# Kernel tuning notes

Measured on AMD Instinct MI355X. Metric: run time of the kernel, lower is better.

## Reference

```python
import jax, jax.numpy as jnp
import numpy as np

B, N, D = 32, 2048, 512

def setup_inputs() -> dict:
    key = jax.random.key(0)
    k1, k2, k3, k4 = jax.random.split(key, 4)
    return {
        "src": jax.random.normal(k1, (B, N, 3), dtype=jnp.float32),
        "tgt": jax.random.normal(k2, (B, N, 3), dtype=jnp.float32),
        "src_embed": jax.random.normal(k3, (B, N, D), dtype=jnp.float32),
        "tgt_embed": jax.random.normal(k4, (B, N, D), dtype=jnp.float32),
    }

def reference(src, tgt, src_embed, tgt_embed):
    # src, tgt: (B, N, 3); src_embed, tgt_embed: (B, N, D)
    d_k = jnp.asarray(src_embed.shape[-1], dtype=src_embed.dtype)
    # attention scores (B, N_src, N_tgt), softmax over tgt points
    scores = jnp.einsum('bnd,bmd->bnm', src_embed, tgt_embed) / jnp.sqrt(d_k)
    pointer = jax.nn.softmax(scores, axis=2)
    # matched = tgt^T @ pointer^T -> (B, 3, N_src)
    matched = jnp.einsum('bmc,bnm->bcn', tgt, pointer)
    src_t = jnp.transpose(src, (0, 2, 1))  # (B, 3, N)
    src_cent = jnp.mean(src_t, axis=2, keepdims=True)        # (B, 3, 1)
    matched_cent = jnp.mean(matched, axis=2, keepdims=True)  # (B, 3, 1)
    src_demean = src_t - src_cent
    matched_demean = matched - matched_cent
    # cross-covariance H: (B, 3, 3)
    H = jnp.einsum('bcn,bdn->bcd', src_demean, matched_demean)
    U, _, Vh = jnp.linalg.svd(H, full_matrices=False)  # square 3x3: reduced == full
    V = jnp.transpose(Vh, (0, 2, 1))
    R = jnp.matmul(V, jnp.transpose(U, (0, 2, 1)))
    det = jnp.linalg.det(R)
    identity = jnp.eye(3, dtype=R.dtype)
    reflect = jnp.diag(jnp.array([1.0, 1.0, -1.0], dtype=R.dtype))
    refl = jnp.where((det >= 0)[:, None, None], identity, reflect)
    R = jnp.matmul(refl, R)
    t = jnp.matmul(-R, src_cent) + matched_cent  # (B, 3, 1)
    t = jnp.transpose(t, (0, 2, 1))              # (B, 1, 3)
    return (R, t)
```

## Files before the change

kernel.cpp:

```cpp
#include <hip/hip_runtime.h>
#include <hip/hip_fp16.h>
#include <math.h>

#define B_ 32
#define N_ 2048
#define D_ 512
#define BN 128
#define NWAVE 8

typedef __attribute__((ext_vector_type(8))) _Float16 f16x8;
typedef __attribute__((ext_vector_type(8))) short s16x8;
typedef __attribute__((ext_vector_type(4))) float f32x4;
typedef __attribute__((ext_vector_type(4))) unsigned int u32x4;

__device__ inline unsigned packh2(float lo, float hi) {
    __half l = __float2half_rn(lo), h = __float2half_rn(hi);
    return (unsigned)__half_as_ushort(l) | ((unsigned)__half_as_ushort(h) << 16);
}
__device__ inline unsigned f2bf(float x) {
    unsigned u = __float_as_uint(x);
    return (u + 0x7FFFu + ((u >> 16) & 1u)) >> 16;
}
__device__ inline float bf2f(unsigned h) { return __uint_as_float(h << 16); }

__global__ __launch_bounds__(256) void prepass_kernel(
    const float* __restrict__ te, u32x4* __restrict__ kp)
{
    const int idx = blockIdx.x * 256 + threadIdx.x;
    const int b   = idx >> 17;
    const int r17 = idx & 131071;
    const int mt  = r17 >> 13;
    const int kt  = (r17 >> 9) & 15;
    const int o16 = r17 & 511;
    const int r   = o16 >> 2;
    const int s   = o16 & 3;
    const int lg  = s ^ ((r >> 1) & 3);
    const float* src = te + (((size_t)b * N_ + mt * 128 + r) * D_ + kt * 32 + lg * 8);
    const float4 f0 = *(const float4*)src;
    const float4 f1 = *(const float4*)(src + 4);
    u32x4 u;
    u[0] = packh2(f0.x, f0.y);
    u[1] = packh2(f0.z, f0.w);
    u[2] = packh2(f1.x, f1.y);
    u[3] = packh2(f1.z, f1.w);
    kp[idx] = u;
}

__global__ __launch_bounds__(512, 2) void attn_fast_kernel(
    const float* __restrict__ src, const float* __restrict__ tgt,
    const float* __restrict__ src_embed, const u32x4* __restrict__ kp,
    double* __restrict__ partials)
{
    __shared__ f16x8 Kbuf[2][512];
    __shared__ float4 TsB[2][BN];
    __shared__ double red[NWAVE][15];

    const int tid  = threadIdx.x;
    const int wv   = tid >> 6;
    const int lane = tid & 63;
    const int lr   = lane & 15;
    const int lg   = lane >> 4;

    const int xcd  = blockIdx.x & 7;
    const int slot = blockIdx.x >> 3;
    const int b    = xcd * 4 + (slot >> 3);
    const int msl  = slot & 7;
    const int n0   = msl * 256;
    const int pblk = b * 8 + msl;

    const int sx   = lg ^ ((lr >> 1) & 3);
    char* KbufB = (char*)&Kbuf[0][0];

    const float QSC = 0.044194173824159216f * 1.4426950408889634f;
    f16x8 Qr[2][16];
#pragma unroll
    for (int qf = 0; qf < 2; ++qf) {
        const int qrow = n0 + wv * 32 + qf * 16 + lr;
        const float* qp = src_embed + ((size_t)b * N_ + qrow) * D_ + lg * 8;
#pragma unroll
        for (int s = 0; s < 16; ++s) {
            const float4 f0 = *(const float4*)(qp + s * 32);
            const float4 f1 = *(const float4*)(qp + s * 32 + 4);
            u32x4 u;
            u[0] = packh2(f0.x * QSC, f0.y * QSC);
            u[1] = packh2(f0.z * QSC, f0.w * QSC);
            u[2] = packh2(f1.x * QSC, f1.y * QSC);
            u[3] = packh2(f1.z * QSC, f1.w * QSC);
            Qr[qf][s] = __builtin_bit_cast(f16x8, u);
        }
    }

#define TILEPTR(mt_, kt_) (kp + ((((size_t)b * 16 + (mt_)) * 16 + (kt_)) << 9) + tid)
#define STAGE(mt_, kt_, bufi_) \
    __builtin_amdgcn_global_load_lds( \
        (const __attribute__((address_space(1))) void*)TILEPTR(mt_, kt_), \
        (__attribute__((address_space(3))) void*)(&Kbuf[bufi_][wv * 64]), 16, 0, 0)

    float m_s[2] = {-1e30f, -1e30f}, l_s[2] = {0.f, 0.f};
    float axs[2] = {0.f, 0.f}, ays[2] = {0.f, 0.f}, azs[2] = {0.f, 0.f};

    STAGE(0, 0, 0);
    if (tid < BN) {
        const float* tp = tgt + ((size_t)b * N_ + tid) * 3;
        TsB[0][tid] = make_float4(tp[0], tp[1], tp[2], 0.f);
    }
    __syncthreads();

    for (int mc = 0; mc < 16; ++mc) {
        f32x4 acc[2][8];
#pragma unroll
        for (int qf = 0; qf < 2; ++qf)
#pragma unroll
            for (int nf = 0; nf < 8; ++nf) acc[qf][nf] = (f32x4){0.f, 0.f, 0.f, 0.f};

        float tv0 = 0.f, tv1 = 0.f, tv2 = 0.f;
#pragma unroll
        for (int kt = 0; kt < 16; ++kt) {
            const int cur = kt & 1;
            if (kt < 15)          { STAGE(mc,     kt + 1, cur ^ 1); }
            else if (mc < 15)     { STAGE(mc + 1, 0,      cur ^ 1); }
            if (kt == 0 && mc < 15 && tid < BN) {
                const float* tp = tgt + ((size_t)b * N_ + (mc + 1) * BN + tid) * 3;
                tv0 = tp[0]; tv1 = tp[1]; tv2 = tp[2];
            }
            const char* base = KbufB + cur * 8192 + lr * 64 + sx * 16;
#pragma unroll
            for (int nf = 0; nf < 8; ++nf) {
                const f16x8 a = *(const f16x8*)(base + nf * 1024);
                acc[0][nf] = __builtin_amdgcn_mfma_f32_16x16x32_f16(a, Qr[0][kt], acc[0][nf], 0, 0, 0);
                acc[1][nf] = __builtin_amdgcn_mfma_f32_16x16x32_f16(a, Qr[1][kt], acc[1][nf], 0, 0, 0);
            }
            if (kt == 0 && mc < 15 && tid < BN)
                TsB[(mc + 1) & 1][tid] = make_float4(tv0, tv1, tv2, 0.f);
            __syncthreads();
        }

        const float4* Ts = TsB[mc & 1];
        float mx0 = -1e30f, mx1 = -1e30f;
#pragma unroll
        for (int nf = 0; nf < 8; ++nf)
#pragma unroll
            for (int r4 = 0; r4 < 4; ++r4) {
                mx0 = fmaxf(mx0, acc[0][nf][r4]);
                mx1 = fmaxf(mx1, acc[1][nf][r4]);
            }
        mx0 = fmaxf(mx0, __shfl_xor(mx0, 16)); mx0 = fmaxf(mx0, __shfl_xor(mx0, 32));
        mx1 = fmaxf(mx1, __shfl_xor(mx1, 16)); mx1 = fmaxf(mx1, __shfl_xor(mx1, 32));
        const float mn0 = fmaxf(m_s[0], mx0), mn1 = fmaxf(m_s[1], mx1);
        const float c0 = exp2f(m_s[0] - mn0), c1 = exp2f(m_s[1] - mn1);
        l_s[0] *= c0; axs[0] *= c0; ays[0] *= c0; azs[0] *= c0; m_s[0] = mn0;
        l_s[1] *= c1; axs[1] *= c1; ays[1] *= c1; azs[1] *= c1; m_s[1] = mn1;
        float l0 = 0.f, x0 = 0.f, y0 = 0.f, z0 = 0.f;
        float l1 = 0.f, x1 = 0.f, y1 = 0.f, z1 = 0.f;
#pragma unroll
        for (int nf = 0; nf < 8; ++nf)
#pragma unroll
            for (int r4 = 0; r4 < 4; ++r4) {
                const float4 tv = Ts[nf * 16 + lg * 4 + r4];
                const float p0 = exp2f(acc[0][nf][r4] - mn0);
                const float p1 = exp2f(acc[1][nf][r4] - mn1);
                l0 += p0; x0 = fmaf(p0, tv.x, x0); y0 = fmaf(p0, tv.y, y0); z0 = fmaf(p0, tv.z, z0);
                l1 += p1; x1 = fmaf(p1, tv.x, x1); y1 = fmaf(p1, tv.y, y1); z1 = fmaf(p1, tv.z, z1);
            }
        l_s[0] += l0; axs[0] += x0; ays[0] += y0; azs[0] += z0;
        l_s[1] += l1; axs[1] += x1; ays[1] += y1; azs[1] += z1;
        __syncthreads();
    }

    double dl[15];
#pragma unroll
    for (int i = 0; i < 15; ++i) dl[i] = 0.0;
#pragma unroll
    for (int qf = 0; qf < 2; ++qf) {
        float lt = l_s[qf], x = axs[qf], y = ays[qf], z = azs[qf];
        lt += __shfl_xor(lt, 16); lt += __shfl_xor(lt, 32);
        x  += __shfl_xor(x, 16);  x  += __shfl_xor(x, 32);
        y  += __shfl_xor(y, 16);  y  += __shfl_xor(y, 32);
        z  += __shfl_xor(z, 16);  z  += __shfl_xor(z, 32);
        if (lg == 0) {
            const int qrow = n0 + wv * 32 + qf * 16 + lr;
            const float* sp = src + ((size_t)b * N_ + qrow) * 3;
            const double inv = 1.0 / (double)lt;
            const double m0d = (double)x * inv, m1d = (double)y * inv, m2d = (double)z * inv;
            const double s0 = sp[0], s1 = sp[1], s2 = sp[2];
            dl[0] += s0;  dl[1] += s1;  dl[2] += s2;
            dl[3] += m0d; dl[4] += m1d; dl[5] += m2d;
            dl[6]  += s0 * m0d; dl[7]  += s0 * m1d; dl[8]  += s0 * m2d;
            dl[9]  += s1 * m0d; dl[10] += s1 * m1d; dl[11] += s1 * m2d;
            dl[12] += s2 * m0d; dl[13] += s2 * m1d; dl[14] += s2 * m2d;
        }
    }
#pragma unroll
    for (int i = 0; i < 15; ++i) {
        double v = dl[i];
        for (int off = 1; off < 64; off <<= 1) v += __shfl_xor(v, off);
        dl[i] = v;
    }
    if (lane == 0) {
#pragma unroll
        for (int i = 0; i < 15; ++i) red[wv][i] = dl[i];
    }
    __syncthreads();
    if (tid < 15) {
        double sum = 0.0;
        for (int w = 0; w < NWAVE; ++w) sum += red[w][tid];
        partials[(size_t)pblk * 15 + tid] = sum;
    }
#undef STAGE
#undef TILEPTR
}

__global__ __launch_bounds__(256, 2) void attn_v2_kernel(
    const float* __restrict__ src, const float* __restrict__ tgt,
    const float* __restrict__ src_embed, const float* __restrict__ tgt_embed,
    double* __restrict__ partials)
{
    __shared__ short Khi_s[128 * 64];
    __shared__ short Klo_s[128 * 64];
    __shared__ float4 Ts4[128];
    __shared__ double red[64][15];

    char* KhiB = (char*)Khi_s;
    char* KloB = (char*)Klo_s;

    const int w    = blockIdx.x;
    const int xcd  = w & 7;
    const int idx  = w >> 3;
    const int b    = xcd * 4 + (idx >> 5);
    const int n0   = (idx & 31) * 64;
    const int blk  = b * 32 + (idx & 31);

    const int tid  = threadIdx.x;
    const int wv   = tid >> 6;
    const int lane = tid & 63;
    const int lr   = lane & 15;
    const int lg   = lane >> 4;
    const unsigned swl = (unsigned)((lr & 7) << 4);

    const float scale = 0.044194173824159216f;
    const float* kbase = tgt_embed + (size_t)b * N_ * D_;

    const int qrow = n0 + wv * 16 + lr;
    const float* qp = src_embed + ((size_t)b * N_ + qrow) * D_ + lg * 8;
    s16x8 qhi[16], qlo[16];
#pragma unroll
    for (int s = 0; s < 16; ++s) {
        const float4 f0 = *reinterpret_cast<const float4*>(qp + s * 32);
        const float4 f1 = *reinterpret_cast<const float4*>(qp + s * 32 + 4);
        const float x[8] = {f0.x, f0.y, f0.z, f0.w, f1.x, f1.y, f1.z, f1.w};
#pragma unroll
        for (int i = 0; i < 8; ++i) {
            const float v = x[i] * scale;
            const unsigned h = f2bf(v);
            qhi[s][i] = (short)h;
            qlo[s][i] = (short)f2bf(v - bf2f(h));
        }
    }

    float m_run = -1e30f, l_run = 0.f, a0 = 0.f, a1 = 0.f, a2 = 0.f;
    const int srow = tid >> 1;
    const int shalf = tid & 1;
    const unsigned swr = (unsigned)((srow & 7) << 4);

    for (int m0 = 0; m0 < N_; m0 += 128) {
        f32x4 acc[8];
#pragma unroll
        for (int nf = 0; nf < 8; ++nf) acc[nf] = (f32x4){0.f, 0.f, 0.f, 0.f};

#pragma unroll
        for (int kt = 0; kt < 8; ++kt) {
            __syncthreads();
            {
                const float* gp = kbase + (size_t)(m0 + srow) * D_ + kt * 64 + shalf * 32;
#pragma unroll
                for (int grp = 0; grp < 4; ++grp) {
                    const float4 fa = *reinterpret_cast<const float4*>(gp + grp * 8);
                    const float4 fb = *reinterpret_cast<const float4*>(gp + grp * 8 + 4);
                    const float x[8] = {fa.x, fa.y, fa.z, fa.w, fb.x, fb.y, fb.z, fb.w};
                    s16x8 hi, lo;
#pragma unroll
                    for (int i = 0; i < 8; ++i) {
                        const unsigned h = f2bf(x[i]);
                        hi[i] = (short)h;
                        lo[i] = (short)f2bf(x[i] - bf2f(h));
                    }
                    const unsigned off = (unsigned)srow * 128u +
                        (((unsigned)(shalf * 64 + grp * 16)) ^ swr);
                    *reinterpret_cast<s16x8*>(KhiB + off) = hi;
                    *reinterpret_cast<s16x8*>(KloB + off) = lo;
                }
                if (kt == 0 && tid < 128) {
                    const float* tp = tgt + ((size_t)b * N_ + m0 + tid) * 3;
                    Ts4[tid] = make_float4(tp[0], tp[1], tp[2], 0.f);
                }
            }
            __syncthreads();
#pragma unroll
            for (int ks = 0; ks < 2; ++ks) {
                const int s = kt * 2 + ks;
                const unsigned kb = ((unsigned)(lg * 16 + ks * 64)) ^ swl;
#pragma unroll
                for (int nf = 0; nf < 8; ++nf) {
                    const unsigned off = (unsigned)(nf * 16 + lr) * 128u + kb;
                    const s16x8 ah = *reinterpret_cast<const s16x8*>(KhiB + off);
                    const s16x8 al = *reinterpret_cast<const s16x8*>(KloB + off);
                    acc[nf] = __builtin_amdgcn_mfma_f32_16x16x32_bf16(ah, qhi[s], acc[nf], 0, 0, 0);
                    acc[nf] = __builtin_amdgcn_mfma_f32_16x16x32_bf16(al, qhi[s], acc[nf], 0, 0, 0);
                    acc[nf] = __builtin_amdgcn_mfma_f32_16x16x32_bf16(ah, qlo[s], acc[nf], 0, 0, 0);
                }
            }
        }

        float mx = -1e30f;
#pragma unroll
        for (int nf = 0; nf < 8; ++nf)
#pragma unroll
            for (int r = 0; r < 4; ++r) mx = fmaxf(mx, acc[nf][r]);
        mx = fmaxf(mx, __shfl_xor(mx, 16));
        mx = fmaxf(mx, __shfl_xor(mx, 32));

        const float mnew = fmaxf(m_run, mx);
        const float corr = __expf(m_run - mnew);
        l_run *= corr; a0 *= corr; a1 *= corr; a2 *= corr;

        float ps = 0.f, p0 = 0.f, p1 = 0.f, p2 = 0.f;
#pragma unroll
        for (int nf = 0; nf < 8; ++nf)
#pragma unroll
            for (int r = 0; r < 4; ++r) {
                const float p = __expf(acc[nf][r] - mnew);
                const int n = nf * 16 + lg * 4 + r;
                const float4 tv = Ts4[n];
                ps += p;
                p0 = fmaf(p, tv.x, p0);
                p1 = fmaf(p, tv.y, p1);
                p2 = fmaf(p, tv.z, p2);
            }
        l_run += ps; a0 += p0; a1 += p1; a2 += p2;
        m_run = mnew;
    }

    l_run += __shfl_xor(l_run, 16); l_run += __shfl_xor(l_run, 32);
    a0 += __shfl_xor(a0, 16); a0 += __shfl_xor(a0, 32);
    a1 += __shfl_xor(a1, 16); a1 += __shfl_xor(a1, 32);
    a2 += __shfl_xor(a2, 16); a2 += __shfl_xor(a2, 32);

    __syncthreads();
    if (lg == 0) {
        const float inv = 1.0f / l_run;
        const double mx0 = (double)(a0 * inv);
        const double mx1 = (double)(a1 * inv);
        const double mx2 = (double)(a2 * inv);
        const float* sp = src + ((size_t)b * N_ + qrow) * 3;
        const double s0 = sp[0], s1 = sp[1], s2 = sp[2];
        double* rp = red[wv * 16 + lr];
        rp[0] = s0;  rp[1] = s1;  rp[2] = s2;
        rp[3] = mx0; rp[4] = mx1; rp[5] = mx2;
        rp[6]  = s0 * mx0; rp[7]  = s0 * mx1; rp[8]  = s0 * mx2;
        rp[9]  = s1 * mx0; rp[10] = s1 * mx1; rp[11] = s1 * mx2;
        rp[12] = s2 * mx0; rp[13] = s2 * mx1; rp[14] = s2 * mx2;
    }
    __syncthreads();
    if (tid < 15) {
        double sum = 0.0;
        for (int j = 0; j < 64; ++j) sum += red[j][tid];
        partials[(size_t)blk * 15 + tid] = sum;
    }
}

__global__ void kabsch_kernel(const double* __restrict__ partials,
                              float* __restrict__ out, int nbb)
{
    const int b = threadIdx.x;
    if (b >= B_) return;

    double acc[15];
#pragma unroll
    for (int i = 0; i < 15; ++i) acc[i] = 0.0;
    for (int rb = 0; rb < nbb; ++rb) {
        const double* p = partials + ((size_t)b * nbb + rb) * 15;
#pragma unroll
        for (int i = 0; i < 15; ++i) acc[i] += p[i];
    }

    const double invN = 1.0 / (double)N_;
    const double S[3] = {acc[0], acc[1], acc[2]};
    const double M[3] = {acc[3], acc[4], acc[5]};
    double H[3][3];
    for (int c = 0; c < 3; ++c)
        for (int d = 0; d < 3; ++d)
            H[c][d] = acc[6 + c * 3 + d] - S[c] * M[d] * invN;

    double A[3][3];
    for (int i = 0; i < 3; ++i)
        for (int j = 0; j < 3; ++j)
            A[i][j] = H[0][i] * H[0][j] + H[1][i] * H[1][j] + H[2][i] * H[2][j];

    double V[3][3] = {{1, 0, 0}, {0, 1, 0}, {0, 0, 1}};
    const int PQ[3][2] = {{0, 1}, {0, 2}, {1, 2}};
    for (int sweep = 0; sweep < 20; ++sweep) {
        const double off = fabs(A[0][1]) + fabs(A[0][2]) + fabs(A[1][2]);
        if (off < 1e-24) break;
        for (int pi = 0; pi < 3; ++pi) {
            const int p = PQ[pi][0], q = PQ[pi][1], rr = 3 - p - q;
            const double apq = A[p][q];
            if (fabs(apq) < 1e-300) continue;
            const double theta = (A[q][q] - A[p][p]) / (2.0 * apq);
            const double tt = (theta >= 0.0 ? 1.0 : -1.0) /
                              (fabs(theta) + sqrt(1.0 + theta * theta));
            const double c = 1.0 / sqrt(1.0 + tt * tt);
            const double sn = tt * c;
            const double app = A[p][p], aqq = A[q][q];
            const double arp = A[rr][p], arq = A[rr][q];
            A[p][p] = app - tt * apq;
            A[q][q] = aqq + tt * apq;
            A[p][q] = A[q][p] = 0.0;
            A[rr][p] = A[p][rr] = c * arp - sn * arq;
            A[rr][q] = A[q][rr] = sn * arp + c * arq;
            for (int k = 0; k < 3; ++k) {
                const double vkp = V[k][p], vkq = V[k][q];
                V[k][p] = c * vkp - sn * vkq;
                V[k][q] = sn * vkp + c * vkq;
            }
        }
    }

    double R[3][3] = {{0, 0, 0}, {0, 0, 0}, {0, 0, 0}};
    for (int i = 0; i < 3; ++i) {
        const double lam = A[i][i];
        const double sig = sqrt(lam > 0.0 ? lam : 0.0);
        const double inv = 1.0 / (sig > 1e-30 ? sig : 1e-30);
        double wv[3];
        for (int c = 0; c < 3; ++c)
            wv[c] = H[c][0] * V[0][i] + H[c][1] * V[1][i] + H[c][2] * V[2][i];
        for (int r = 0; r < 3; ++r)
            for (int c = 0; c < 3; ++c)
                R[r][c] += V[r][i] * wv[c] * inv;
    }

    const double det =
        R[0][0] * (R[1][1] * R[2][2] - R[1][2] * R[2][1]) -
        R[0][1] * (R[1][0] * R[2][2] - R[1][2] * R[2][0]) +
        R[0][2] * (R[1][0] * R[2][1] - R[1][1] * R[2][0]);
    if (det < 0.0) {
        R[2][0] = -R[2][0]; R[2][1] = -R[2][1]; R[2][2] = -R[2][2];
    }

    double t[3];
    for (int c = 0; c < 3; ++c)
        t[c] = M[c] * invN -
               (R[c][0] * S[0] + R[c][1] * S[1] + R[c][2] * S[2]) * invN;

    for (int r = 0; r < 3; ++r)
        for (int c = 0; c < 3; ++c)
            out[(size_t)b * 9 + r * 3 + c] = (float)R[r][c];
    for (int c = 0; c < 3; ++c)
        out[(size_t)B_ * 9 + (size_t)b * 3 + c] = (float)t[c];
}

extern "C" void kernel_launch(void* const* d_in, const int* in_sizes, int n_in,
                              void* d_out, int out_size, void* d_ws, size_t ws_size,
                              hipStream_t stream) {
    const float* src = (const float*)d_in[0];
    const float* tgt = (const float*)d_in[1];
    const float* se  = (const float*)d_in[2];
    const float* te  = (const float*)d_in[3];
    float* out = (float*)d_out;

    const size_t KP_OFF = 32768;
    const size_t need = KP_OFF + (size_t)B_ * N_ * D_ * 2;

    if (ws_size >= need) {
        u32x4* kp = (u32x4*)((char*)d_ws + KP_OFF);
        prepass_kernel<<<dim3(16384), dim3(256), 0, stream>>>(te, kp);
        attn_fast_kernel<<<dim3(256), dim3(512), 0, stream>>>(
            src, tgt, se, kp, (double*)d_ws);
        kabsch_kernel<<<dim3(1), dim3(64), 0, stream>>>((double*)d_ws, out, 8);
    } else {
        attn_v2_kernel<<<dim3(1024), dim3(256), 0, stream>>>(
            src, tgt, se, te, (double*)d_ws);
        kabsch_kernel<<<dim3(1), dim3(64), 0, stream>>>((double*)d_ws, out, 32);
    }
}
```

Measured before the change: 267.1 us.

## Restructure attention kernel into 4-slot async K ring with smaller blocks

Replaces the 512-thread double-buffered attention kernel with a 256-thread kernel that streams K tiles through a 4-slot LDS ring, prefetching three tiles ahead. It waits on explicit vmcnt counts with one barrier per step instead of two full syncthreads. All tgt coordinates for the batch are preloaded into LDS once, and the grid doubles to 512 blocks of 128 query rows. Partials are now stored as float rather than double, which costs some precision in the cross-covariance sums.

After: 227.1 us. -15.0%, faster.

```diff
diff --git a/kernel.cpp b/kernel.cpp
--- a/kernel.cpp
+++ b/kernel.cpp
@@ -5,8 +5,7 @@
 #define B_ 32
 #define N_ 2048
 #define D_ 512
-#define BN 128
-#define NWAVE 8
+#define NT 256
 
 typedef __attribute__((ext_vector_type(8))) _Float16 f16x8;
 typedef __attribute__((ext_vector_type(8))) short s16x8;
@@ -46,30 +45,29 @@
     kp[idx] = u;
 }
 
-__global__ __launch_bounds__(512, 2) void attn_fast_kernel(
+__global__ __launch_bounds__(NT, 2) void attn_pipe_kernel(
     const float* __restrict__ src, const float* __restrict__ tgt,
     const float* __restrict__ src_embed, const u32x4* __restrict__ kp,
-    double* __restrict__ partials)
+    float* __restrict__ partials)
 {
-    __shared__ f16x8 Kbuf[2][512];
-    __shared__ float4 TsB[2][BN];
-    __shared__ double red[NWAVE][15];
+    __shared__ f16x8 ring[4][512];
+    __shared__ float4 Ts4[N_];
+    __shared__ double red[4][15];
 
     const int tid  = threadIdx.x;
     const int wv   = tid >> 6;
     const int lane = tid & 63;
     const int lr   = lane & 15;
     const int lg   = lane >> 4;
+    const int sxb  = (lg ^ ((lr >> 1) & 3)) << 4;
+    char* ringB = (char*)&ring[0][0];
 
     const int xcd  = blockIdx.x & 7;
-    const int slot = blockIdx.x >> 3;
-    const int b    = xcd * 4 + (slot >> 3);
-    const int msl  = slot & 7;
-    const int n0   = msl * 256;
-    const int pblk = b * 8 + msl;
-
-    const int sx   = lg ^ ((lr >> 1) & 3);
-    char* KbufB = (char*)&Kbuf[0][0];
+    const int idx  = blockIdx.x >> 3;
+    const int b    = xcd * 4 + (idx >> 4);
+    const int msl  = idx & 15;
+    const int n0   = msl * 128;
+    const int pblk = b * 16 + msl;
 
     const float QSC = 0.044194173824159216f * 1.4426950408889634f;
     f16x8 Qr[2][16];
@@ -89,60 +87,73 @@
             Qr[qf][s] = __builtin_bit_cast(f16x8, u);
         }
     }
-
-#define TILEPTR(mt_, kt_) (kp + ((((size_t)b * 16 + (mt_)) * 16 + (kt_)) << 9) + tid)
-#define STAGE(mt_, kt_, bufi_) \
-    __builtin_amdgcn_global_load_lds( \
-        (const __attribute__((address_space(1))) void*)TILEPTR(mt_, kt_), \
-        (__attribute__((address_space(3))) void*)(&Kbuf[bufi_][wv * 64]), 16, 0, 0)
+    {
+        const float* tb = tgt + (size_t)b * N_ * 3;
+#pragma unroll
+        for (int i = 0; i < 8; ++i) {
+            const int r = tid + i * 256;
+            Ts4[r] = make_float4(tb[r * 3], tb[r * 3 + 1], tb[r * 3 + 2], 0.f);
+        }
+    }
+    __syncthreads();
+
+#define STAGE(mc_, kt_, slot_) do {                                            \
+    const u32x4* _g = kp + ((((size_t)b * 16 + (mc_)) * 16 + (kt_)) << 9);     \
+    __builtin_amdgcn_global_load_lds(                                          \
+        (const __attribute__((address_space(1))) void*)(_g + tid),             \
+        (__attribute__((address_space(3))) void*)(&ring[slot_][wv * 64]),      \
+        16, 0, 0);                                                             \
+    __builtin_amdgcn_global_load_lds(                                          \
+        (const __attribute__((address_space(1))) void*)(_g + 256 + tid),       \
+        (__attribute__((address_space(3))) void*)(&ring[slot_][256 + wv * 64]),\
+        16, 0, 0);                                                             \
+} while (0)
+
+    STAGE(0, 0, 0);
+    STAGE(0, 1, 1);
+    STAGE(0, 2, 2);
 
     float m_s[2] = {-1e30f, -1e30f}, l_s[2] = {0.f, 0.f};
     float axs[2] = {0.f, 0.f}, ays[2] = {0.f, 0.f}, azs[2] = {0.f, 0.f};
 
-    STAGE(0, 0, 0);
-    if (tid < BN) {
-        const float* tp = tgt + ((size_t)b * N_ + tid) * 3;
-        TsB[0][tid] = make_float4(tp[0], tp[1], tp[2], 0.f);
-    }
-    __syncthreads();
-
     for (int mc = 0; mc < 16; ++mc) {
-        f32x4 acc[2][8];
-#pragma unroll
-        for (int qf = 0; qf < 2; ++qf)
-#pragma unroll
-            for (int nf = 0; nf < 8; ++nf) acc[qf][nf] = (f32x4){0.f, 0.f, 0.f, 0.f};
-
-        float tv0 = 0.f, tv1 = 0.f, tv2 = 0.f;
+        f32x4 acc0[8], acc1[8];
+#pragma unroll
+        for (int nf = 0; nf < 8; ++nf) {
+            acc0[nf] = (f32x4){0.f, 0.f, 0.f, 0.f};
+            acc1[nf] = (f32x4){0.f, 0.f, 0.f, 0.f};
+        }
+
 #pragma unroll
         for (int kt = 0; kt < 16; ++kt) {
-            const int cur = kt & 1;
-            if (kt < 15)          { STAGE(mc,     kt + 1, cur ^ 1); }
-            else if (mc < 15)     { STAGE(mc + 1, 0,      cur ^ 1); }
-            if (kt == 0 && mc < 15 && tid < BN) {
-                const float* tp = tgt + ((size_t)b * N_ + (mc + 1) * BN + tid) * 3;
-                tv0 = tp[0]; tv1 = tp[1]; tv2 = tp[2];
-            }
-            const char* base = KbufB + cur * 8192 + lr * 64 + sx * 16;
+            const int t = (mc << 4) + kt;
+            if (mc == 15 && kt >= 14) {
+                asm volatile("s_waitcnt vmcnt(0)" ::: "memory");
+            } else {
+                asm volatile("s_waitcnt vmcnt(4)" ::: "memory");
+            }
+            __builtin_amdgcn_s_barrier();
+            if (t <= 252) {
+                const int tn = t + 3;
+                STAGE(tn >> 4, tn & 15, tn & 3);
+            }
+            const char* abase = ringB + ((t & 3) << 13) + lr * 64 + sxb;
 #pragma unroll
             for (int nf = 0; nf < 8; ++nf) {
-                const f16x8 a = *(const f16x8*)(base + nf * 1024);
-                acc[0][nf] = __builtin_amdgcn_mfma_f32_16x16x32_f16(a, Qr[0][kt], acc[0][nf], 0, 0, 0);
-                acc[1][nf] = __builtin_amdgcn_mfma_f32_16x16x32_f16(a, Qr[1][kt], acc[1][nf], 0, 0, 0);
-            }
-            if (kt == 0 && mc < 15 && tid < BN)
-                TsB[(mc + 1) & 1][tid] = make_float4(tv0, tv1, tv2, 0.f);
-            __syncthreads();
-        }
-
-        const float4* Ts = TsB[mc & 1];
+                const f16x8 a = *(const f16x8*)(abase + nf * 1024);
+                acc0[nf] = __builtin_amdgcn_mfma_f32_16x16x32_f16(a, Qr[0][kt], acc0[nf], 0, 0, 0);
+                acc1[nf] = __builtin_amdgcn_mfma_f32_16x16x32_f16(a, Qr[1][kt], acc1[nf], 0, 0, 0);
+            }
+        }
+
+        const float4* Ts = &Ts4[mc * 128];
         float mx0 = -1e30f, mx1 = -1e30f;
 #pragma unroll
         for (int nf = 0; nf < 8; ++nf)
 #pragma unroll
             for (int r4 = 0; r4 < 4; ++r4) {
-                mx0 = fmaxf(mx0, acc[0][nf][r4]);
-                mx1 = fmaxf(mx1, acc[1][nf][r4]);
+                mx0 = fmaxf(mx0, acc0[nf][r4]);
+                mx1 = fmaxf(mx1, acc1[nf][r4]);
             }
         mx0 = fmaxf(mx0, __shfl_xor(mx0, 16)); mx0 = fmaxf(mx0, __shfl_xor(mx0, 32));
         mx1 = fmaxf(mx1, __shfl_xor(mx1, 16)); mx1 = fmaxf(mx1, __shfl_xor(mx1, 32));
@@ -157,15 +168,15 @@
 #pragma unroll
             for (int r4 = 0; r4 < 4; ++r4) {
                 const float4 tv = Ts[nf * 16 + lg * 4 + r4];
-                const float p0 = exp2f(acc[0][nf][r4] - mn0);
-                const float p1 = exp2f(acc[1][nf][r4] - mn1);
+                const float p0 = exp2f(acc0[nf][r4] - mn0);
+                const float p1 = exp2f(acc1[nf][r4] - mn1);
                 l0 += p0; x0 = fmaf(p0, tv.x, x0); y0 = fmaf(p0, tv.y, y0); z0 = fmaf(p0, tv.z, z0);
                 l1 += p1; x1 = fmaf(p1, tv.x, x1); y1 = fmaf(p1, tv.y, y1); z1 = fmaf(p1, tv.z, z1);
             }
         l_s[0] += l0; axs[0] += x0; ays[0] += y0; azs[0] += z0;
         l_s[1] += l1; axs[1] += x1; ays[1] += y1; azs[1] += z1;
-        __syncthreads();
-    }
+    }
+#undef STAGE
 
     double dl[15];
 #pragma unroll
@@ -203,17 +214,15 @@
     __syncthreads();
     if (tid < 15) {
         double sum = 0.0;
-        for (int w = 0; w < NWAVE; ++w) sum += red[w][tid];
-        partials[(size_t)pblk * 15 + tid] = sum;
-    }
-#undef STAGE
-#undef TILEPTR
+        for (int w = 0; w < 4; ++w) sum += red[w][tid];
+        partials[(size_t)pblk * 15 + tid] = (float)sum;
+    }
 }
 
 __global__ __launch_bounds__(256, 2) void attn_v2_kernel(
     const float* __restrict__ src, const float* __restrict__ tgt,
     const float* __restrict__ src_embed, const float* __restrict__ tgt_embed,
-    double* __restrict__ partials)
+    float* __restrict__ partials)
 {
     __shared__ short Khi_s[128 * 64];
     __shared__ short Klo_s[128 * 64];
@@ -364,11 +373,11 @@
     if (tid < 15) {
         double sum = 0.0;
         for (int j = 0; j < 64; ++j) sum += red[j][tid];
-        partials[(size_t)blk * 15 + tid] = sum;
-    }
-}
-
-__global__ void kabsch_kernel(const double* __restrict__ partials,
+        partials[(size_t)blk * 15 + tid] = (float)sum;
+    }
+}
+
+__global__ void kabsch_kernel(const float* __restrict__ partials,
                               float* __restrict__ out, int nbb)
 {
     const int b = threadIdx.x;
@@ -378,9 +387,9 @@
 #pragma unroll
     for (int i = 0; i < 15; ++i) acc[i] = 0.0;
     for (int rb = 0; rb < nbb; ++rb) {
-        const double* p = partials + ((size_t)b * nbb + rb) * 15;
-#pragma unroll
-        for (int i = 0; i < 15; ++i) acc[i] += p[i];
+        const float* p = partials + ((size_t)b * nbb + rb) * 15;
+#pragma unroll
+        for (int i = 0; i < 15; ++i) acc[i] += (double)p[i];
     }
 
     const double invN = 1.0 / (double)N_;
@@ -473,12 +482,12 @@
     if (ws_size >= need) {
         u32x4* kp = (u32x4*)((char*)d_ws + KP_OFF);
         prepass_kernel<<<dim3(16384), dim3(256), 0, stream>>>(te, kp);
-        attn_fast_kernel<<<dim3(256), dim3(512), 0, stream>>>(
-            src, tgt, se, kp, (double*)d_ws);
-        kabsch_kernel<<<dim3(1), dim3(64), 0, stream>>>((double*)d_ws, out, 8);
+        attn_pipe_kernel<<<dim3(512), dim3(NT), 0, stream>>>(
+            src, tgt, se, kp, (float*)d_ws);
+        kabsch_kernel<<<dim3(1), dim3(64), 0, stream>>>((float*)d_ws, out, 16);
     } else {
         attn_v2_kernel<<<dim3(1024), dim3(256), 0, stream>>>(
-            src, tgt, se, te, (double*)d_ws);
-        kabsch_kernel<<<dim3(1), dim3(64), 0, stream>>>((double*)d_ws, out, 32);
-    }
-}
+            src, tgt, se, te, (float*)d_ws);
+        kabsch_kernel<<<dim3(1), dim3(64), 0, stream>>>((float*)d_ws, out, 32);
+    }
+}
```
